# Kernel optimization log

Measured on AMD Instinct MI355X. Metric: run time of the kernel, lower is better.

Reference implementation:

```python
import jax, jax.numpy as jnp
import numpy as np

N = 20000           # graph nodes == vocab_size
E_RAND = 160000     # random edges (avg degree 8)
E = E_RAND + N      # + self loops (dgl.add_self_loop)
B, S, D = 16, 512, 768
IN_DIM, HID, HEADS = 4, 16, 8
GRID = 10010
NEG_SLOPE = 0.2


def _zero_row0(t):
    # padding_idx=0 in nn.Embedding -> row 0 is zeros
    return t.at[0].set(0.0)


def setup_inputs() -> dict:
    key = jax.random.key(0)
    ks = jax.random.split(key, 20)
    self_loops = jnp.arange(N, dtype=jnp.int64 if jax.config.x64_enabled else jnp.int32)
    edge_src = jax.random.randint(ks[0], (E,), 0, N).at[E_RAND:].set(self_loops)
    edge_dst = jax.random.randint(ks[1], (E,), 0, N).at[E_RAND:].set(self_loops)
    inp = {
        "trj_token": jax.random.randint(ks[2], (B, S), 0, N),
        "min_list": jax.random.randint(ks[3], (B, S), 0, 1441),
        "weekday_list": jax.random.randint(ks[4], (B, S), 0, 8),
        "day_list": jax.random.randint(ks[5], (B, S), 0, 367),
        "grid_list": jax.random.randint(ks[6], (B, S), 0, GRID),
        "poi_list": jax.random.randint(ks[7], (B, S), 0, 5),
        "edge_src": edge_src,
        "edge_dst": edge_dst,
        "feature": jax.random.normal(ks[8], (N, IN_DIM), jnp.float32),
        "W_src1": jax.random.normal(ks[9], (IN_DIM, HEADS, HID), jnp.float32) * 0.3,
        "W_dst1": jax.random.normal(ks[10], (IN_DIM, HEADS, HID), jnp.float32) * 0.3,
        "attn1": jax.random.normal(ks[11], (HEADS, HID), jnp.float32) * 0.3,
        "W_src2": jax.random.normal(ks[12], (HEADS * HID, 1, D), jnp.float32) * 0.05,
        "W_dst2": jax.random.normal(ks[13], (HEADS * HID, 1, D), jnp.float32) * 0.05,
        "attn2": jax.random.normal(ks[14], (1, D), jnp.float32) * 0.05,
        "grid_table": _zero_row0(jax.random.normal(ks[15], (GRID, D), jnp.float32)),
        "daytime_table": _zero_row0(jax.random.normal(ks[16], (1441, D), jnp.float32)),
        "weekday_table": _zero_row0(jax.random.normal(ks[17], (8, D), jnp.float32)),
        "day_table": _zero_row0(jax.random.normal(ks[18], (367, D), jnp.float32)),
    }
    return inp


def gatv2_layer(x, es, ed, W_s, W_d, attn):
    # GATv2: score_e = attn . leaky_relu(Wsrc x[src] + Wdst x[dst]); edge-softmax over dst
    hs = jnp.einsum('nd,dhf->nhf', x, W_s)           # [N,H,F]
    hd = jnp.einsum('nd,dhf->nhf', x, W_d)           # [N,H,F]
    e = jax.nn.leaky_relu(hs[es] + hd[ed], NEG_SLOPE)  # [E,H,F]
    score = jnp.einsum('ehf,hf->eh', e, attn)        # [E,H]
    m = jax.lax.stop_gradient(jax.ops.segment_max(score, ed, num_segments=N))
    ex = jnp.exp(score - m[ed])
    denom = jax.ops.segment_sum(ex, ed, num_segments=N)  # [N,H]
    alpha = ex / denom[ed]                           # [E,H]
    msg = alpha[..., None] * hs[es]                  # [E,H,F]
    return jax.ops.segment_sum(msg, ed, num_segments=N)  # [N,H,F]


def positional_embedding(seq_len, d_model):
    pos = jnp.arange(seq_len, dtype=jnp.float32)[:, None]
    div = jnp.exp(jnp.arange(0, d_model, 2, dtype=jnp.float32) * (-np.log(10000.0) / d_model))
    pe = jnp.zeros((seq_len, d_model), jnp.float32)
    pe = pe.at[:, 0::2].set(jnp.sin(pos * div))
    pe = pe.at[:, 1::2].set(jnp.cos(pos * div))
    return pe[None]  # [1,S,D]


def reference(trj_token, min_list, weekday_list, day_list, grid_list, poi_list,
              edge_src, edge_dst, feature,
              W_src1, W_dst1, attn1, W_src2, W_dst2, attn2,
              grid_table, daytime_table, weekday_table, day_table):
    # GAT2: two GATv2 layers over the road-network graph
    h1 = gatv2_layer(feature, edge_src, edge_dst, W_src1, W_dst1, attn1)   # [N,8,16]
    h1 = jax.nn.elu(h1.reshape(N, HEADS * HID))                            # concat heads
    h2 = gatv2_layer(h1, edge_src, edge_dst, W_src2, W_dst2, attn2)        # [N,1,768]
    node_emb = h2[:, 0, :]                                                 # [N,768]

    token = node_emb[trj_token]                                            # [B,S,D]
    time_emb = (weekday_table[weekday_list]
                + daytime_table[min_list]
                + day_table[day_list])
    grid_emb = grid_table[grid_list]
    pe = positional_embedding(trj_token.shape[1], D)
    return pe + token + time_emb + grid_emb
```

## Files before the change

kernel.cpp:

```cpp
#include <hip/hip_runtime.h>
#include <hip/hip_bf16.h>

#define N_NODES 20000
#define N_EDGES 180000
#define D_OUT   768
#define D_H1    128
#define B_SZ    16
#define S_LEN   512
#define NEG_SLOPE_C 0.2f

__device__ __forceinline__ float leaky1(float x){ return x >= 0.0f ? x : NEG_SLOPE_C * x; }
__device__ __forceinline__ unsigned short f2bf(float x){
  union { __hip_bfloat16 h; unsigned short u; } v; v.h = __float2bfloat16(x); return v.u;
}
__device__ __forceinline__ float bf2f(unsigned short u){
  return __uint_as_float(((unsigned)u) << 16);
}
__device__ __forceinline__ float4 bf4_to_f4(ushort4 u){
  return make_float4(bf2f(u.x), bf2f(u.y), bf2f(u.z), bf2f(u.w));
}

__global__ void k_count(const int* __restrict__ ed, int* __restrict__ deg){
  int e = blockIdx.x*256 + threadIdx.x;
  if(e < N_EDGES) atomicAdd(&deg[ed[e]], 1);
}

__global__ void k_scan(const int* __restrict__ deg, int* __restrict__ row_ptr, int* __restrict__ cursor){
  __shared__ int part[256];
  int t = threadIdx.x;
  const int CH = (N_NODES + 255) / 256;
  int base = t * CH;
  int s = 0;
  for(int i=0;i<CH;i++){ int n = base+i; if(n < N_NODES) s += deg[n]; }
  part[t] = s;
  __syncthreads();
  for(int off=1; off<256; off<<=1){
    int v = (t >= off) ? part[t-off] : 0;
    __syncthreads();
    part[t] += v;
    __syncthreads();
  }
  int run = (t==0) ? 0 : part[t-1];
  for(int i=0;i<CH;i++){
    int n = base+i;
    if(n < N_NODES){ row_ptr[n] = run; cursor[n] = run; run += deg[n]; }
  }
  if(t == 255) row_ptr[N_NODES] = run;
}

__global__ void k_scatter(const int* __restrict__ ed, int* __restrict__ cursor, int* __restrict__ eidx){
  int e = blockIdx.x*256 + threadIdx.x;
  if(e < N_EDGES){
    int pos = atomicAdd(&cursor[ed[e]], 1);
    eidx[pos] = e;
  }
}

__global__ void k_gemm1(const float* __restrict__ feat, const float* __restrict__ Ws,
                        const float* __restrict__ Wd,
                        unsigned short* __restrict__ hs1, unsigned short* __restrict__ hd1){
  int idx = blockIdx.x*256 + threadIdx.x;
  if(idx >= N_NODES*D_H1) return;
  int n = idx >> 7, hf = idx & 127;
  float f0 = feat[n*4+0], f1 = feat[n*4+1], f2 = feat[n*4+2], f3 = feat[n*4+3];
  hs1[idx] = f2bf(f0*Ws[hf] + f1*Ws[128+hf] + f2*Ws[256+hf] + f3*Ws[384+hf]);
  hd1[idx] = f2bf(f0*Wd[hf] + f1*Wd[128+hf] + f2*Wd[256+hf] + f3*Wd[384+hf]);
}

__global__ void k_fused1(const unsigned short* __restrict__ hs1, const unsigned short* __restrict__ hd1,
                         const int* __restrict__ es, const int* __restrict__ row_ptr,
                         const int* __restrict__ eidx, const float* __restrict__ attn1,
                         float* __restrict__ h1){
  int node = blockIdx.x*4 + (threadIdx.x >> 6);
  int l = threadIdx.x & 63;
  if(node >= N_NODES) return;
  int rp = row_ptr[node], re = row_ptr[node+1];
  float hda = bf2f(hd1[(size_t)node*D_H1 + l]);
  float hdb = bf2f(hd1[(size_t)node*D_H1 + 64 + l]);
  float awa = attn1[l], awb = attn1[64 + l];
  float m0 = -INFINITY, m1 = -INFINITY;
  float d0 = 0.f, d1 = 0.f, a0 = 0.f, a1 = 0.f;
  for(int k=rp; k<re; k++){
    int e = eidx[k]; int s = es[e];
    float hsa = bf2f(hs1[(size_t)s*D_H1 + l]);
    float hsb = bf2f(hs1[(size_t)s*D_H1 + 64 + l]);
    float t0 = leaky1(hsa + hda) * awa;
    float t1 = leaky1(hsb + hdb) * awb;
    #pragma unroll
    for(int off=1; off<16; off<<=1){
      t0 += __shfl_xor(t0, off, 64);
      t1 += __shfl_xor(t1, off, 64);
    }
    float mn0 = fmaxf(m0, t0), mn1 = fmaxf(m1, t1);
    float r0 = expf(m0 - mn0), r1 = expf(m1 - mn1);
    float w0 = expf(t0 - mn0), w1 = expf(t1 - mn1);
    d0 = d0*r0 + w0;           d1 = d1*r1 + w1;
    a0 = a0*r0 + w0*hsa;       a1 = a1*r1 + w1*hsb;
    m0 = mn0;                  m1 = mn1;
  }
  float v0 = a0 / d0, v1 = a1 / d1;
  h1[(size_t)node*D_H1 + l]      = v0 > 0.f ? v0 : expm1f(v0);
  h1[(size_t)node*D_H1 + 64 + l] = v1 > 0.f ? v1 : expm1f(v1);
}

__global__ __launch_bounds__(256,2) void k_gemm2(const float* __restrict__ h1,
                        const float* __restrict__ Ws, const float* __restrict__ Wd,
                        unsigned short* __restrict__ hs2, unsigned short* __restrict__ hd2){
  __shared__ float At[8][136];
  __shared__ float Bs[8][128];
  __shared__ float Bd[8][128];
  int m0 = blockIdx.x * 128;
  int c0 = blockIdx.y * 128;
  int tx = threadIdx.x;
  int cg = tx & 15;
  int rg = tx >> 4;
  float acc_s[8][8], acc_d[8][8];
  #pragma unroll
  for(int i=0;i<8;i++)
    #pragma unroll
    for(int j=0;j<8;j++){ acc_s[i][j]=0.f; acc_d[i][j]=0.f; }

  for(int k0=0; k0<D_H1; k0+=8){
    __syncthreads();
    {
      int r = tx >> 1, kh = tx & 1;
      int row = m0 + r;
      float4 a = (row < N_NODES) ? *(const float4*)&h1[(size_t)row*D_H1 + k0 + kh*4]
                                 : make_float4(0.f,0.f,0.f,0.f);
      At[kh*4+0][r] = a.x; At[kh*4+1][r] = a.y; At[kh*4+2][r] = a.z; At[kh*4+3][r] = a.w;
    }
    {
      int kk = tx >> 5, c4 = (tx & 31) * 4;
      *(float4*)&Bs[kk][c4] = *(const float4*)&Ws[(size_t)(k0+kk)*D_OUT + c0 + c4];
      *(float4*)&Bd[kk][c4] = *(const float4*)&Wd[(size_t)(k0+kk)*D_OUT + c0 + c4];
    }
    __syncthreads();
    #pragma unroll
    for(int kk=0;kk<8;kk++){
      float4 a0 = *(const float4*)&At[kk][rg*8];
      float4 a1 = *(const float4*)&At[kk][rg*8+4];
      float4 b0 = *(const float4*)&Bs[kk][cg*4];
      float4 b1 = *(const float4*)&Bs[kk][64+cg*4];
      float4 e0 = *(const float4*)&Bd[kk][cg*4];
      float4 e1 = *(const float4*)&Bd[kk][64+cg*4];
      float av[8]  = {a0.x,a0.y,a0.z,a0.w,a1.x,a1.y,a1.z,a1.w};
      float bsv[8] = {b0.x,b0.y,b0.z,b0.w,b1.x,b1.y,b1.z,b1.w};
      float bdv[8] = {e0.x,e0.y,e0.z,e0.w,e1.x,e1.y,e1.z,e1.w};
      #pragma unroll
      for(int i=0;i<8;i++)
        #pragma unroll
        for(int j=0;j<8;j++){
          acc_s[i][j] += av[i]*bsv[j];
          acc_d[i][j] += av[i]*bdv[j];
        }
    }
  }
  #pragma unroll
  for(int i=0;i<8;i++){
    int row = m0 + rg*8 + i;
    if(row < N_NODES){
      size_t base = (size_t)row*D_OUT + c0;
      ushort4 u;
      u.x=f2bf(acc_s[i][0]); u.y=f2bf(acc_s[i][1]); u.z=f2bf(acc_s[i][2]); u.w=f2bf(acc_s[i][3]);
      *(ushort4*)&hs2[base + cg*4] = u;
      u.x=f2bf(acc_s[i][4]); u.y=f2bf(acc_s[i][5]); u.z=f2bf(acc_s[i][6]); u.w=f2bf(acc_s[i][7]);
      *(ushort4*)&hs2[base + 64 + cg*4] = u;
      u.x=f2bf(acc_d[i][0]); u.y=f2bf(acc_d[i][1]); u.z=f2bf(acc_d[i][2]); u.w=f2bf(acc_d[i][3]);
      *(ushort4*)&hd2[base + cg*4] = u;
      u.x=f2bf(acc_d[i][4]); u.y=f2bf(acc_d[i][5]); u.z=f2bf(acc_d[i][6]); u.w=f2bf(acc_d[i][7]);
      *(ushort4*)&hd2[base + 64 + cg*4] = u;
    }
  }
}

__global__ void k_fused2(const unsigned short* __restrict__ hs2, const unsigned short* __restrict__ hd2,
                         const int* __restrict__ es, const int* __restrict__ row_ptr,
                         const int* __restrict__ eidx, const float* __restrict__ attn2,
                         float* __restrict__ h2){
  int node = blockIdx.x*4 + (threadIdx.x >> 6);
  int l = threadIdx.x & 63;
  if(node >= N_NODES) return;
  int rp = row_ptr[node], re = row_ptr[node+1];
  const ushort4* pd = (const ushort4*)(hd2 + (size_t)node*D_OUT);
  const float4*  pa = (const float4*)attn2;
  float4 hd0 = bf4_to_f4(pd[l]), hd1v = bf4_to_f4(pd[64+l]), hd2v = bf4_to_f4(pd[128+l]);
  float4 aw0 = pa[l], aw1 = pa[64+l], aw2 = pa[128+l];
  float m = -INFINITY, den = 0.f;
  float4 ac0 = make_float4(0,0,0,0), ac1 = make_float4(0,0,0,0), ac2 = make_float4(0,0,0,0);
  for(int k=rp; k<re; k++){
    int e = eidx[k]; int s = es[e];
    const ushort4* ps = (const ushort4*)(hs2 + (size_t)s*D_OUT);
    float4 v0 = bf4_to_f4(ps[l]), v1 = bf4_to_f4(ps[64+l]), v2 = bf4_to_f4(ps[128+l]);
    float sc = leaky1(v0.x+hd0.x)*aw0.x + leaky1(v0.y+hd0.y)*aw0.y
             + leaky1(v0.z+hd0.z)*aw0.z + leaky1(v0.w+hd0.w)*aw0.w
             + leaky1(v1.x+hd1v.x)*aw1.x + leaky1(v1.y+hd1v.y)*aw1.y
             + leaky1(v1.z+hd1v.z)*aw1.z + leaky1(v1.w+hd1v.w)*aw1.w
             + leaky1(v2.x+hd2v.x)*aw2.x + leaky1(v2.y+hd2v.y)*aw2.y
             + leaky1(v2.z+hd2v.z)*aw2.z + leaky1(v2.w+hd2v.w)*aw2.w;
    #pragma unroll
    for(int off=1; off<64; off<<=1) sc += __shfl_xor(sc, off, 64);
    float mn = fmaxf(m, sc);
    float r = expf(m - mn);
    float w = expf(sc - mn);
    den = den*r + w;
    ac0.x = ac0.x*r + w*v0.x; ac0.y = ac0.y*r + w*v0.y;
    ac0.z = ac0.z*r + w*v0.z; ac0.w = ac0.w*r + w*v0.w;
    ac1.x = ac1.x*r + w*v1.x; ac1.y = ac1.y*r + w*v1.y;
    ac1.z = ac1.z*r + w*v1.z; ac1.w = ac1.w*r + w*v1.w;
    ac2.x = ac2.x*r + w*v2.x; ac2.y = ac2.y*r + w*v2.y;
    ac2.z = ac2.z*r + w*v2.z; ac2.w = ac2.w*r + w*v2.w;
    m = mn;
  }
  float rd = 1.f/den;
  float4* po = (float4*)(h2 + (size_t)node*D_OUT);
  ac0.x*=rd; ac0.y*=rd; ac0.z*=rd; ac0.w*=rd;
  ac1.x*=rd; ac1.y*=rd; ac1.z*=rd; ac1.w*=rd;
  ac2.x*=rd; ac2.y*=rd; ac2.z*=rd; ac2.w*=rd;
  po[l] = ac0; po[64+l] = ac1; po[128+l] = ac2;
}

__global__ __launch_bounds__(192) void k_out(const float* __restrict__ h2,
    const int* __restrict__ tok, const int* __restrict__ mins, const int* __restrict__ wkd,
    const int* __restrict__ dayl, const int* __restrict__ grd,
    const float* __restrict__ grid_t, const float* __restrict__ dayt_t,
    const float* __restrict__ week_t, const float* __restrict__ day_t,
    float* __restrict__ out){
  int bs = blockIdx.x;
  int t  = threadIdx.x;
  int s  = bs & (S_LEN-1);
  int tk = tok[bs], mn = mins[bs], wk = wkd[bs], dy = dayl[bs], gr = grd[bs];
  float4 r = ((const float4*)(h2 + (size_t)tk*D_OUT))[t];
  float4 v;
  v = ((const float4*)(week_t + (size_t)wk*D_OUT))[t]; r.x+=v.x; r.y+=v.y; r.z+=v.z; r.w+=v.w;
  v = ((const float4*)(dayt_t + (size_t)mn*D_OUT))[t]; r.x+=v.x; r.y+=v.y; r.z+=v.z; r.w+=v.w;
  v = ((const float4*)(day_t  + (size_t)dy*D_OUT))[t]; r.x+=v.x; r.y+=v.y; r.z+=v.z; r.w+=v.w;
  v = ((const float4*)(grid_t + (size_t)gr*D_OUT))[t]; r.x+=v.x; r.y+=v.y; r.z+=v.z; r.w+=v.w;
  const float K = 0.011992630692677313f;
  float d0 = expf(-K * (float)(4*t));
  float d1 = expf(-K * (float)(4*t+2));
  float sf = (float)s;
  r.x += sinf(sf*d0); r.y += cosf(sf*d0);
  r.z += sinf(sf*d1); r.w += cosf(sf*d1);
  ((float4*)(out + (size_t)bs*D_OUT))[t] = r;
}

extern "C" void kernel_launch(void* const* d_in, const int* in_sizes, int n_in,
                              void* d_out, int out_size, void* d_ws, size_t ws_size,
                              hipStream_t stream) {
  const int*   trj   = (const int*)  d_in[0];
  const int*   mins  = (const int*)  d_in[1];
  const int*   wkd   = (const int*)  d_in[2];
  const int*   dayl  = (const int*)  d_in[3];
  const int*   grd   = (const int*)  d_in[4];
  const int*   es    = (const int*)  d_in[6];
  const int*   ed    = (const int*)  d_in[7];
  const float* feat  = (const float*)d_in[8];
  const float* Ws1   = (const float*)d_in[9];
  const float* Wd1   = (const float*)d_in[10];
  const float* attn1 = (const float*)d_in[11];
  const float* Ws2   = (const float*)d_in[12];
  const float* Wd2   = (const float*)d_in[13];
  const float* attn2 = (const float*)d_in[14];
  const float* gridt = (const float*)d_in[15];
  const float* daytt = (const float*)d_in[16];
  const float* weekt = (const float*)d_in[17];
  const float* dayt  = (const float*)d_in[18];
  float* out = (float*)d_out;

  char* ws = (char*)d_ws;
  size_t off = 0;
  auto alloc = [&](size_t bytes)->char*{
    char* p = ws + off;
    off += bytes;
    off = (off + 255) & ~(size_t)255;
    return p;
  };
  unsigned short* hs1 = (unsigned short*)alloc((size_t)N_NODES*D_H1*2);
  unsigned short* hd1 = (unsigned short*)alloc((size_t)N_NODES*D_H1*2);
  float*          h1  = (float*)         alloc((size_t)N_NODES*D_H1*4);
  unsigned short* hs2 = (unsigned short*)alloc((size_t)N_NODES*D_OUT*2);
  unsigned short* hd2 = (unsigned short*)alloc((size_t)N_NODES*D_OUT*2);
  float*          h2  = (float*)         alloc((size_t)N_NODES*D_OUT*4);
  int* deg      = (int*)alloc((size_t)N_NODES*4);
  int* row_ptr  = (int*)alloc((size_t)(N_NODES+1)*4);
  int* cursor   = (int*)alloc((size_t)N_NODES*4);
  int* eidx     = (int*)alloc((size_t)N_EDGES*4);

  hipMemsetAsync(deg, 0, (size_t)N_NODES*4, stream);
  k_count  <<<(N_EDGES+255)/256, 256, 0, stream>>>(ed, deg);
  k_scan   <<<1, 256, 0, stream>>>(deg, row_ptr, cursor);
  k_scatter<<<(N_EDGES+255)/256, 256, 0, stream>>>(ed, cursor, eidx);

  k_gemm1 <<<(N_NODES*D_H1)/256, 256, 0, stream>>>(feat, Ws1, Wd1, hs1, hd1);
  k_fused1<<<(N_NODES+3)/4, 256, 0, stream>>>(hs1, hd1, es, row_ptr, eidx, attn1, h1);

  dim3 g2((N_NODES+127)/128, D_OUT/128);
  k_gemm2 <<<g2, 256, 0, stream>>>(h1, Ws2, Wd2, hs2, hd2);
  k_fused2<<<(N_NODES+3)/4, 256, 0, stream>>>(hs2, hd2, es, row_ptr, eidx, attn2, h2);

  k_out<<<B_SZ*S_LEN, 192, 0, stream>>>(h2, trj, mins, wkd, dayl, grd,
                                        gridt, daytt, weekt, dayt, out);
}
```

Measured before the change: 422.1 us.

## Use bf16 MFMA for layer-2 projection GEMM with transposed bf16 weights

Replaces the fp32 LDS-tiled SIMT GEMM for the second GATv2 projection with a register-only MFMA 16x16x32 bf16 kernel. The first layer's output h1 is now stored in bf16, and a small prep kernel transposes and converts the layer-2 weights to bf16 each call. This targets the FMA-bound fp32 GEMM and halves the h1 traffic. The cost is lower input precision and scalar 2-byte output stores in place of vectorized ones.

```diff
diff --git a/kernel.cpp b/kernel.cpp
--- a/kernel.cpp
+++ b/kernel.cpp
@@ -8,6 +8,9 @@
 #define B_SZ    16
 #define S_LEN   512
 #define NEG_SLOPE_C 0.2f
+
+typedef __attribute__((ext_vector_type(8))) short bf16x8;
+typedef __attribute__((ext_vector_type(4))) float f32x4;
 
 __device__ __forceinline__ float leaky1(float x){ return x >= 0.0f ? x : NEG_SLOPE_C * x; }
 __device__ __forceinline__ unsigned short f2bf(float x){
@@ -70,7 +73,7 @@
 __global__ void k_fused1(const unsigned short* __restrict__ hs1, const unsigned short* __restrict__ hd1,
                          const int* __restrict__ es, const int* __restrict__ row_ptr,
                          const int* __restrict__ eidx, const float* __restrict__ attn1,
-                         float* __restrict__ h1){
+                         unsigned short* __restrict__ h1){
   int node = blockIdx.x*4 + (threadIdx.x >> 6);
   int l = threadIdx.x & 63;
   if(node >= N_NODES) return;
@@ -99,76 +102,74 @@
     m0 = mn0;                  m1 = mn1;
   }
   float v0 = a0 / d0, v1 = a1 / d1;
-  h1[(size_t)node*D_H1 + l]      = v0 > 0.f ? v0 : expm1f(v0);
-  h1[(size_t)node*D_H1 + 64 + l] = v1 > 0.f ? v1 : expm1f(v1);
-}
-
-__global__ __launch_bounds__(256,2) void k_gemm2(const float* __restrict__ h1,
-                        const float* __restrict__ Ws, const float* __restrict__ Wd,
+  v0 = v0 > 0.f ? v0 : expm1f(v0);
+  v1 = v1 > 0.f ? v1 : expm1f(v1);
+  h1[(size_t)node*D_H1 + l]      = f2bf(v0);
+  h1[(size_t)node*D_H1 + 64 + l] = f2bf(v1);
+}
+
+__global__ void k_wprep(const float* __restrict__ Ws, const float* __restrict__ Wd,
+                        unsigned short* __restrict__ WtS, unsigned short* __restrict__ WtD){
+  int i = blockIdx.x*256 + threadIdx.x;
+  if(i >= D_OUT*D_H1) return;
+  int c = i >> 7, k = i & 127;
+  WtS[i] = f2bf(Ws[(size_t)k*D_OUT + c]);
+  WtD[i] = f2bf(Wd[(size_t)k*D_OUT + c]);
+}
+
+__global__ __launch_bounds__(256) void k_gemm2m(const unsigned short* __restrict__ h1b,
+                        const unsigned short* __restrict__ WtS, const unsigned short* __restrict__ WtD,
                         unsigned short* __restrict__ hs2, unsigned short* __restrict__ hd2){
-  __shared__ float At[8][136];
-  __shared__ float Bs[8][128];
-  __shared__ float Bd[8][128];
-  int m0 = blockIdx.x * 128;
-  int c0 = blockIdx.y * 128;
-  int tx = threadIdx.x;
-  int cg = tx & 15;
-  int rg = tx >> 4;
-  float acc_s[8][8], acc_d[8][8];
+  int wave = threadIdx.x >> 6, lane = threadIdx.x & 63;
+  int wr = wave >> 1, wc = wave & 1;
+  int m0 = blockIdx.x*64 + wr*32;
+  int c0 = blockIdx.y*128 + wc*64;
+  int lr = lane & 15, lk = lane >> 4;
+
+  f32x4 acc[2][4][2];
   #pragma unroll
-  for(int i=0;i<8;i++)
-    #pragma unroll
-    for(int j=0;j<8;j++){ acc_s[i][j]=0.f; acc_d[i][j]=0.f; }
-
-  for(int k0=0; k0<D_H1; k0+=8){
-    __syncthreads();
-    {
-      int r = tx >> 1, kh = tx & 1;
-      int row = m0 + r;
-      float4 a = (row < N_NODES) ? *(const float4*)&h1[(size_t)row*D_H1 + k0 + kh*4]
-                                 : make_float4(0.f,0.f,0.f,0.f);
-      At[kh*4+0][r] = a.x; At[kh*4+1][r] = a.y; At[kh*4+2][r] = a.z; At[kh*4+3][r] = a.w;
+  for(int a=0;a<2;a++)
+    #pragma unroll
+    for(int j=0;j<4;j++)
+      #pragma unroll
+      for(int mmat=0;mmat<2;mmat++)
+        acc[a][j][mmat] = (f32x4){0.f,0.f,0.f,0.f};
+
+  int ra0 = m0 + lr;      if(ra0 > N_NODES-1) ra0 = N_NODES-1;
+  int ra1 = m0 + 16 + lr; if(ra1 > N_NODES-1) ra1 = N_NODES-1;
+  const unsigned short* pa0 = h1b + (size_t)ra0*D_H1 + lk*8;
+  const unsigned short* pa1 = h1b + (size_t)ra1*D_H1 + lk*8;
+
+  #pragma unroll
+  for(int t=0;t<4;t++){
+    bf16x8 a0 = *(const bf16x8*)(pa0 + t*32);
+    bf16x8 a1 = *(const bf16x8*)(pa1 + t*32);
+    #pragma unroll
+    for(int j=0;j<4;j++){
+      size_t bo = (size_t)(c0 + j*16 + lr)*D_H1 + t*32 + lk*8;
+      bf16x8 bs = *(const bf16x8*)(WtS + bo);
+      bf16x8 bd = *(const bf16x8*)(WtD + bo);
+      acc[0][j][0] = __builtin_amdgcn_mfma_f32_16x16x32_bf16(a0, bs, acc[0][j][0], 0, 0, 0);
+      acc[1][j][0] = __builtin_amdgcn_mfma_f32_16x16x32_bf16(a1, bs, acc[1][j][0], 0, 0, 0);
+      acc[0][j][1] = __builtin_amdgcn_mfma_f32_16x16x32_bf16(a0, bd, acc[0][j][1], 0, 0, 0);
+      acc[1][j][1] = __builtin_amdgcn_mfma_f32_16x16x32_bf16(a1, bd, acc[1][j][1], 0, 0, 0);
     }
-    {
-      int kk = tx >> 5, c4 = (tx & 31) * 4;
-      *(float4*)&Bs[kk][c4] = *(const float4*)&Ws[(size_t)(k0+kk)*D_OUT + c0 + c4];
-      *(float4*)&Bd[kk][c4] = *(const float4*)&Wd[(size_t)(k0+kk)*D_OUT + c0 + c4];
-    }
-    __syncthreads();
-    #pragma unroll
-    for(int kk=0;kk<8;kk++){
-      float4 a0 = *(const float4*)&At[kk][rg*8];
-      float4 a1 = *(const float4*)&At[kk][rg*8+4];
-      float4 b0 = *(const float4*)&Bs[kk][cg*4];
-      float4 b1 = *(const float4*)&Bs[kk][64+cg*4];
-      float4 e0 = *(const float4*)&Bd[kk][cg*4];
-      float4 e1 = *(const float4*)&Bd[kk][64+cg*4];
-      float av[8]  = {a0.x,a0.y,a0.z,a0.w,a1.x,a1.y,a1.z,a1.w};
-      float bsv[8] = {b0.x,b0.y,b0.z,b0.w,b1.x,b1.y,b1.z,b1.w};
-      float bdv[8] = {e0.x,e0.y,e0.z,e0.w,e1.x,e1.y,e1.z,e1.w};
-      #pragma unroll
-      for(int i=0;i<8;i++)
+  }
+
+  #pragma unroll
+  for(int a=0;a<2;a++){
+    #pragma unroll
+    for(int r=0;r<4;r++){
+      int row = m0 + a*16 + lk*4 + r;
+      if(row < N_NODES){
+        size_t base = (size_t)row*D_OUT;
         #pragma unroll
-        for(int j=0;j<8;j++){
-          acc_s[i][j] += av[i]*bsv[j];
-          acc_d[i][j] += av[i]*bdv[j];
+        for(int j=0;j<4;j++){
+          int col = c0 + j*16 + lr;
+          hs2[base + col] = f2bf(acc[a][j][0][r]);
+          hd2[base + col] = f2bf(acc[a][j][1][r]);
         }
-    }
-  }
-  #pragma unroll
-  for(int i=0;i<8;i++){
-    int row = m0 + rg*8 + i;
-    if(row < N_NODES){
-      size_t base = (size_t)row*D_OUT + c0;
-      ushort4 u;
-      u.x=f2bf(acc_s[i][0]); u.y=f2bf(acc_s[i][1]); u.z=f2bf(acc_s[i][2]); u.w=f2bf(acc_s[i][3]);
-      *(ushort4*)&hs2[base + cg*4] = u;
-      u.x=f2bf(acc_s[i][4]); u.y=f2bf(acc_s[i][5]); u.z=f2bf(acc_s[i][6]); u.w=f2bf(acc_s[i][7]);
-      *(ushort4*)&hs2[base + 64 + cg*4] = u;
-      u.x=f2bf(acc_d[i][0]); u.y=f2bf(acc_d[i][1]); u.z=f2bf(acc_d[i][2]); u.w=f2bf(acc_d[i][3]);
-      *(ushort4*)&hd2[base + cg*4] = u;
-      u.x=f2bf(acc_d[i][4]); u.y=f2bf(acc_d[i][5]); u.z=f2bf(acc_d[i][6]); u.w=f2bf(acc_d[i][7]);
-      *(ushort4*)&hd2[base + 64 + cg*4] = u;
+      }
     }
   }
 }
@@ -277,7 +278,9 @@
   };
   unsigned short* hs1 = (unsigned short*)alloc((size_t)N_NODES*D_H1*2);
   unsigned short* hd1 = (unsigned short*)alloc((size_t)N_NODES*D_H1*2);
-  float*          h1  = (float*)         alloc((size_t)N_NODES*D_H1*4);
+  unsigned short* h1  = (unsigned short*)alloc((size_t)N_NODES*D_H1*2);
+  unsigned short* WtS = (unsigned short*)alloc((size_t)D_OUT*D_H1*2);
+  unsigned short* WtD = (unsigned short*)alloc((size_t)D_OUT*D_H1*2);
   unsigned short* hs2 = (unsigned short*)alloc((size_t)N_NODES*D_OUT*2);
   unsigned short* hd2 = (unsigned short*)alloc((size_t)N_NODES*D_OUT*2);
   float*          h2  = (float*)         alloc((size_t)N_NODES*D_OUT*4);
@@ -294,8 +297,9 @@
   k_gemm1 <<<(N_NODES*D_H1)/256, 256, 0, stream>>>(feat, Ws1, Wd1, hs1, hd1);
   k_fused1<<<(N_NODES+3)/4, 256, 0, stream>>>(hs1, hd1, es, row_ptr, eidx, attn1, h1);
 
-  dim3 g2((N_NODES+127)/128, D_OUT/128);
-  k_gemm2 <<<g2, 256, 0, stream>>>(h1, Ws2, Wd2, hs2, hd2);
+  k_wprep <<<(D_OUT*D_H1+255)/256, 256, 0, stream>>>(Ws2, Wd2, WtS, WtD);
+  dim3 g2((N_NODES+63)/64, D_OUT/128);
+  k_gemm2m<<<g2, 256, 0, stream>>>(h1, WtS, WtD, hs2, hd2);
   k_fused2<<<(N_NODES+3)/4, 256, 0, stream>>>(hs2, hd2, es, row_ptr, eidx, attn2, h2);
 
   k_out<<<B_SZ*S_LEN, 192, 0, stream>>>(h2, trj, mins, wkd, dayl, grd,
```

Result: faster. 374.9 us (-11.2%).
